# Kernel optimization log

Measured on AMD Instinct MI355X. Metric: run time of the kernel, lower is better.

The kernel has to match this reference:

```python
import jax, jax.numpy as jnp
import numpy as np

N, F, OUT = 8192, 256, 256


def setup_inputs() -> dict:
    key = jax.random.key(0)
    ks = jax.random.split(key, 8)
    s = 1.0 / np.sqrt(F)
    return {
        "features": jax.random.normal(ks[0], (N, F), jnp.float32),
        "key_features": jax.random.normal(ks[1], (N, F), jnp.float32),
        "adj_matrix": jax.random.uniform(ks[2], (N, N), jnp.float32),
        "W_d": jax.random.normal(ks[3], (2 * F, F), jnp.float32) * (1.0 / np.sqrt(2 * F)),
        "b_d": jnp.zeros((F,), jnp.float32),
        "W_o": jax.random.normal(ks[4], (F, OUT), jnp.float32) * s,
        "b_o": jnp.zeros((OUT,), jnp.float32),
        "W_a": jax.random.normal(ks[5], (F, F), jnp.float32) * s,
        "b_a": jnp.zeros((F,), jnp.float32),
        "W_ao": jax.random.normal(ks[6], (F, OUT), jnp.float32) * s,
        "b_ao": jnp.zeros((OUT,), jnp.float32),
    }


def reference(features, key_features, adj_matrix, W_d, b_d, W_o, b_o, W_a, b_a, W_ao, b_ao):
    n = features.shape[0]
    # masked softmax over rows; self-loop (diagonal) masked out
    neg = jnp.asarray(-1e9, adj_matrix.dtype)
    logits = adj_matrix * 5.0 + jnp.eye(n, dtype=adj_matrix.dtype) * neg
    a = jax.nn.softmax(logits, axis=-1)  # [N, N]
    # sum_j a_ij * concat(x_i, x_j) == concat(x_i * rowsum_i, (A @ X)_i)
    rowsum = jnp.sum(a, axis=-1, keepdims=True)  # == 1, kept for faithfulness
    agg = a @ features  # [N, F]
    neigh = jnp.concatenate([features * rowsum, agg], axis=-1)  # [N, 2F]
    neigh_distill = neigh @ W_d + b_d
    feature_updated = jnp.tanh((features - neigh_distill) @ W_o + b_o)
    # aggregate branch (withAgg=True)
    key_agg = (a @ key_features) @ W_a + b_a
    feature_aggregate = jnp.tanh((key_features + key_agg) @ W_ao + b_ao)
    return (feature_updated, feature_aggregate)
```

## Files before the change

kernel.cpp:

```cpp
#include <hip/hip_runtime.h>
#include <stdint.h>
#include <math.h>


typedef __attribute__((ext_vector_type(4)))  short bf16x4_t;
typedef __attribute__((ext_vector_type(8)))  short bf16x8_t;
typedef __attribute__((ext_vector_type(4)))  float f32x4_t;
typedef __attribute__((ext_vector_type(16))) float f32x16_t;

#define MFMA32(A, B, C) __builtin_amdgcn_mfma_f32_32x32x16_bf16(A, B, C, 0, 0, 0)
#define MFMA16(A, B, C) __builtin_amdgcn_mfma_f32_16x16x32_bf16(A, B, C, 0, 0, 0)

__device__ __forceinline__ unsigned short f2bf(float x) {
    union { float f; unsigned u; } c; c.f = x;
    unsigned u = c.u;
    return (unsigned short)((u + 0x7fffu + ((u >> 16) & 1u)) >> 16);
}
__device__ __forceinline__ unsigned pack2bf(float a, float b) {
    return (unsigned)f2bf(a) | ((unsigned)f2bf(b) << 16);
}
__device__ __forceinline__ float bflo(unsigned u) {
    union { unsigned u; float f; } c; c.u = u << 16; return c.f;
}
__device__ __forceinline__ float bfhi(unsigned u) {
    union { unsigned u; float f; } c; c.u = u & 0xffff0000u; return c.f;
}

__global__ __launch_bounds__(256) void transpose_f32_bf16(
    const float* __restrict__ src, unsigned short* __restrict__ dst, int R, int C)
{
    __shared__ float tile[32][33];
    const int x  = threadIdx.x & 31;
    const int y4 = (threadIdx.x >> 5) * 4;
    const int r0 = blockIdx.x * 32;
    const int c0 = blockIdx.y * 32;
#pragma unroll
    for (int i = 0; i < 4; ++i)
        tile[y4 + i][x] = src[(size_t)(r0 + y4 + i) * C + c0 + x];
    __syncthreads();
#pragma unroll
    for (int i = 0; i < 4; ++i)
        dst[(size_t)(c0 + y4 + i) * R + r0 + x] = f2bf(tile[x][y4 + i]);
}

__global__ __launch_bounds__(256) void pack_half(
    const float* __restrict__ src, unsigned* __restrict__ dst)
{
    const int idx = blockIdx.x * 256 + threadIdx.x;
    const int row = idx >> 7, cp = idx & 127;
    float2 v = *(const float2*)(src + (size_t)row * 256 + cp * 2);
    dst[(size_t)row * 256 + cp] = pack2bf(v.x, v.y);
}

__global__ __launch_bounds__(256) void compose1(
    const float* __restrict__ W_d, const float* __restrict__ W_o,
    unsigned short* __restrict__ W1t)
{
    __shared__ float wrow[256];
    const int k = blockIdx.x, t = threadIdx.x;
    wrow[t] = W_d[(size_t)k * 256 + t];
    __syncthreads();
    float acc = 0.f;
#pragma unroll 8
    for (int m = 0; m < 256; ++m) acc = fmaf(wrow[m], W_o[(size_t)m * 256 + t], acc);
    const float v = (k < 256 ? W_o[(size_t)k * 256 + t] : 0.f) - acc;
    W1t[(size_t)t * 512 + k] = f2bf(v);
}

__global__ __launch_bounds__(256) void compose2(
    const float* __restrict__ W_a, const float* __restrict__ W_ao,
    unsigned short* __restrict__ W2t)
{
    __shared__ float wrow[256];
    const int k = blockIdx.x, t = threadIdx.x;
    float v;
    if (k < 256) {
        v = W_ao[(size_t)k * 256 + t];
    } else {
        wrow[t] = W_a[(size_t)(k - 256) * 256 + t];
        __syncthreads();
        float acc = 0.f;
#pragma unroll 8
        for (int m = 0; m < 256; ++m) acc = fmaf(wrow[m], W_ao[(size_t)m * 256 + t], acc);
        v = acc;
    }
    W2t[(size_t)t * 512 + k] = f2bf(v);
}

__global__ __launch_bounds__(256) void biasC(
    const float* __restrict__ b_d, const float* __restrict__ b_o,
    const float* __restrict__ b_a, const float* __restrict__ b_ao,
    const float* __restrict__ W_o, const float* __restrict__ W_ao,
    float* __restrict__ c1, float* __restrict__ c2)
{
    const int t = threadIdx.x;
    float a1 = 0.f, a2 = 0.f;
#pragma unroll 8
    for (int m = 0; m < 256; ++m) {
        a1 = fmaf(b_d[m], W_o [(size_t)m * 256 + t], a1);
        a2 = fmaf(b_a[m], W_ao[(size_t)m * 256 + t], a2);
    }
    c1[t] = b_o[t] - a1;
    c2[t] = b_ao[t] + a2;
}

#define ROWS 128
#define KSLICE 2048
#define NIT 64
#define NCH 16
#define ASTRIDE 36

__global__ __launch_bounds__(1024) void exp_gemm(
    const float* __restrict__ adj, const unsigned short* __restrict__ Xt,
    unsigned* __restrict__ UpartB, float* __restrict__ sSp)
{
    __shared__ unsigned short sA[2][4][ROWS * ASTRIDE];

    const int t = threadIdx.x;
    const int w = t >> 6, lane = t & 63, q = lane >> 5, l31 = lane & 31;
    const int rb = blockIdx.x >> 2, h = blockIdx.x & 3;
    const int row0 = rb * ROWS, kbase = h * KSLICE;

    const int srow = t >> 3, skoff = (t & 7) * 4;
    const int sgrow = row0 + srow;
    const float* adj_row = adj + (size_t)sgrow * 8192 + kbase + skoff;
    const int swoff = srow * ASTRIDE + skoff;

    const unsigned short* bptr = Xt + (size_t)(w * 32 + l31) * 8192 + kbase + q * 8;

    float rs = 0.f;
    f32x16_t acc[4];
#pragma unroll
    for (int mt = 0; mt < 4; ++mt)
#pragma unroll
        for (int e = 0; e < 16; ++e) acc[mt][e] = 0.f;

    bf16x8_t bq[4][2];
    float4 qaA[4], qaB[4];

    auto stageChunk = [&](int cidx, const float4 (&qa)[4], int buf) {
        unsigned short* sb = &sA[buf][0][0] + swoff;
#pragma unroll
        for (int ks = 0; ks < 4; ++ks) {
            const float4 v = qa[ks];
            float e0 = __expf(5.f * v.x);
            float e1 = __expf(5.f * v.y);
            float e2 = __expf(5.f * v.z);
            float e3 = __expf(5.f * v.w);
            const int gk = kbase + (cidx * 4 + ks) * 32 + skoff;
            if (gk + 0 == sgrow) e0 = 0.f;
            if (gk + 1 == sgrow) e1 = 0.f;
            if (gk + 2 == sgrow) e2 = 0.f;
            if (gk + 3 == sgrow) e3 = 0.f;
            rs += (e0 + e1) + (e2 + e3);
            uint2 p; p.x = pack2bf(e0, e1); p.y = pack2bf(e2, e3);
            *(uint2*)(sb + ks * (ROWS * ASTRIDE)) = p;
        }
    };

    auto phase = [&](int c, float4 (&qaPre)[4], const float4 (&qaStg)[4], int buf) {
        if (c + 2 < NCH) {
#pragma unroll
            for (int ks = 0; ks < 4; ++ks)
                qaPre[ks] = *(const float4*)(adj_row + (size_t)((c + 2) * 4 + ks) * 32);
        }
        if (c + 1 < NCH) stageChunk(c + 1, qaStg, buf ^ 1);
#pragma unroll
        for (int u = 0; u < 4; ++u) {
            const int j = c * 4 + u;
            int jn = j + 2; if (jn >= NIT) jn = 0;
            bq[(u + 2) & 3][0] = *(const bf16x8_t*)(bptr + (size_t)jn * 32);
            bq[(u + 2) & 3][1] = *(const bf16x8_t*)(bptr + (size_t)jn * 32 + 16);
            const unsigned short* sa = &sA[buf][u][0] + l31 * ASTRIDE + q * 8;
#pragma unroll
            for (int s = 0; s < 2; ++s)
#pragma unroll
                for (int mt = 0; mt < 4; ++mt) {
                    const unsigned short* p = sa + mt * (32 * ASTRIDE) + s * 16;
                    bf16x4_t lo = *(const bf16x4_t*)p;
                    bf16x4_t hi = *(const bf16x4_t*)(p + 4);
                    bf16x8_t a = __builtin_shufflevector(lo, hi, 0, 1, 2, 3, 4, 5, 6, 7);
                    acc[mt] = MFMA32(a, bq[u][s], acc[mt]);
                }
        }
        asm volatile("s_waitcnt lgkmcnt(0)\n\ts_barrier" ::: "memory");
    };

#pragma unroll
    for (int ks = 0; ks < 4; ++ks)
        qaA[ks] = *(const float4*)(adj_row + (size_t)ks * 32);
#pragma unroll
    for (int ks = 0; ks < 4; ++ks)
        qaB[ks] = *(const float4*)(adj_row + (size_t)(4 + ks) * 32);
    stageChunk(0, qaA, 0);
    bq[0][0] = *(const bf16x8_t*)(bptr + 0);
    bq[0][1] = *(const bf16x8_t*)(bptr + 16);
    bq[1][0] = *(const bf16x8_t*)(bptr + 32);
    bq[1][1] = *(const bf16x8_t*)(bptr + 48);
    asm volatile("s_waitcnt lgkmcnt(0)\n\ts_barrier" ::: "memory");

    for (int c0 = 0; c0 < NCH; c0 += 2) {
        phase(c0,     qaA, qaB, 0);
        phase(c0 + 1, qaB, qaA, 1);
    }

    rs += __shfl_xor(rs, 1);
    rs += __shfl_xor(rs, 2);
    rs += __shfl_xor(rs, 4);
    if ((t & 7) == 0) sSp[h * 8192 + sgrow] = rs;

    unsigned* up = UpartB + (((size_t)h * 64 + rb) * 16 + w) * 2048 + lane;
#pragma unroll
    for (int mt = 0; mt < 4; ++mt)
#pragma unroll
        for (int ip = 0; ip < 8; ++ip)
            up[(size_t)(mt * 8 + ip) * 64] = pack2bf(acc[mt][2 * ip], acc[mt][2 * ip + 1]);
}

__global__ __launch_bounds__(256) void finalize_agg(
    const unsigned* __restrict__ UpartB, const float* __restrict__ sSp,
    unsigned* __restrict__ XcatN, unsigned* __restrict__ Kcat)
{
    __shared__ float sT[128][65];
    __shared__ float sInv[128];

    const int t = threadIdx.x;
    const int rb = blockIdx.x >> 3, wp = blockIdx.x & 7;
    const int row0 = rb * 128;

    if (t < 128) {
        const int r = row0 + t;
        sInv[t] = 1.f / (sSp[r] + sSp[8192 + r] + sSp[16384 + r] + sSp[24576 + r]);
    }

    const int i = t >> 3;
    const int l0 = (t & 7) * 8;
    const int mt = i >> 3, ip = i & 7;
    const int qq = l0 >> 5;
    const int rlo = mt * 32 + 2 * (ip & 1) + 8 * (ip >> 1) + 4 * qq;
    const int cbase = l0 & 31;

#pragma unroll
    for (int wi = 0; wi < 2; ++wi) {
        const int wv = wp * 2 + wi;
        float lo[8], hi[8];
#pragma unroll
        for (int j = 0; j < 8; ++j) { lo[j] = 0.f; hi[j] = 0.f; }
#pragma unroll
        for (int h = 0; h < 4; ++h) {
            const unsigned* src = UpartB + (((size_t)h * 64 + rb) * 16 + wv) * 2048
                                  + (size_t)i * 64 + l0;
            const uint4 v0 = *(const uint4*)(src);
            const uint4 v1 = *(const uint4*)(src + 4);
            const unsigned vv[8] = { v0.x, v0.y, v0.z, v0.w, v1.x, v1.y, v1.z, v1.w };
#pragma unroll
            for (int j = 0; j < 8; ++j) { lo[j] += bflo(vv[j]); hi[j] += bfhi(vv[j]); }
        }
#pragma unroll
        for (int j = 0; j < 8; ++j) {
            sT[rlo][wi * 32 + cbase + j]     = lo[j];
            sT[rlo + 1][wi * 32 + cbase + j] = hi[j];
        }
    }
    __syncthreads();

    const int row = t >> 1, cg = (t & 1) * 32;
    const float inv = sInv[row];
    unsigned outv[16];
#pragma unroll
    for (int j = 0; j < 16; ++j)
        outv[j] = pack2bf(sT[row][cg + 2 * j] * inv, sT[row][cg + 2 * j + 1] * inv);
    unsigned* dst = (wp < 4 ? XcatN : Kcat)
                    + (size_t)(row0 + row) * 256 + 128 + (wp & 3) * 32 + (cg >> 1);
#pragma unroll
    for (int j = 0; j < 4; ++j)
        *(uint4*)(dst + 4 * j) = *(const uint4*)(outv + 4 * j);
}

__global__ __launch_bounds__(256) void gemm_out(
    const unsigned short* __restrict__ Aa, const unsigned short* __restrict__ Wta,
    const float* __restrict__ ca,
    const unsigned short* __restrict__ Ab, const unsigned short* __restrict__ Wtb,
    const float* __restrict__ cb,
    float* __restrict__ outa, float* __restrict__ outb)
{
    __shared__ unsigned short sAm[16 * ASTRIDE];
    __shared__ unsigned short sB[256 * ASTRIDE];
    __shared__ float sBias[256];

    const int bid = blockIdx.x;
    const int prob = bid >> 9, tile = bid & 511;
    const unsigned short* A  = prob ? Ab  : Aa;
    const unsigned short* Wt = prob ? Wtb : Wta;
    const float* cvec        = prob ? cb  : ca;
    float* out               = prob ? outb : outa;

    const int t = threadIdx.x, w = t >> 6, lane = t & 63;
    const int m_lo = lane & 15, quad = lane >> 4;
    const int row0 = tile * 16;
    sBias[t] = cvec[t];

    f32x4_t acc[4];
#pragma unroll
    for (int b = 0; b < 4; ++b)
#pragma unroll
        for (int e = 0; e < 4; ++e) acc[b][e] = 0.f;

    for (int ks = 0; ks < 16; ++ks) {
        const int k0 = ks * 32;
        __syncthreads();
        if (t < 64) {
            bf16x8_t v = *(const bf16x8_t*)(A + (size_t)(row0 + (t >> 2)) * 512 + k0 + (t & 3) * 8);
            unsigned short* d = &sAm[(t >> 2) * ASTRIDE + (t & 3) * 8];
            *(bf16x4_t*)d       = __builtin_shufflevector(v, v, 0, 1, 2, 3);
            *(bf16x4_t*)(d + 4) = __builtin_shufflevector(v, v, 4, 5, 6, 7);
        }
        {
            const unsigned short* src = Wt + (size_t)t * 512 + k0;
            unsigned short* d = &sB[t * ASTRIDE];
#pragma unroll
            for (int j = 0; j < 4; ++j) {
                bf16x8_t v = *(const bf16x8_t*)(src + j * 8);
                *(bf16x4_t*)(d + j * 8)     = __builtin_shufflevector(v, v, 0, 1, 2, 3);
                *(bf16x4_t*)(d + j * 8 + 4) = __builtin_shufflevector(v, v, 4, 5, 6, 7);
            }
        }
        __syncthreads();
        bf16x8_t a0;
        {
            const unsigned short* p = &sAm[m_lo * ASTRIDE + quad * 8];
            bf16x4_t lo = *(const bf16x4_t*)p, hi = *(const bf16x4_t*)(p + 4);
            a0 = __builtin_shufflevector(lo, hi, 0, 1, 2, 3, 4, 5, 6, 7);
        }
#pragma unroll
        for (int nt = 0; nt < 4; ++nt) {
            const unsigned short* p = &sB[(w * 64 + nt * 16 + m_lo) * ASTRIDE + quad * 8];
            bf16x4_t lo = *(const bf16x4_t*)p, hi = *(const bf16x4_t*)(p + 4);
            bf16x8_t b = __builtin_shufflevector(lo, hi, 0, 1, 2, 3, 4, 5, 6, 7);
            acc[nt] = MFMA16(a0, b, acc[nt]);
        }
    }

#pragma unroll
    for (int nt = 0; nt < 4; ++nt) {
        const int col = w * 64 + nt * 16 + m_lo;
#pragma unroll
        for (int r = 0; r < 4; ++r) {
            const int row = row0 + quad * 4 + r;
            out[(size_t)row * 256 + col] = tanhf(acc[nt][r] + sBias[col]);
        }
    }
}

extern "C" void kernel_launch(void* const* d_in, const int* in_sizes, int n_in,
                              void* d_out, int out_size, void* d_ws, size_t ws_size,
                              hipStream_t stream) {
    const float* features = (const float*)d_in[0];
    const float* key      = (const float*)d_in[1];
    const float* adj      = (const float*)d_in[2];
    const float* W_d  = (const float*)d_in[3];
    const float* b_d  = (const float*)d_in[4];
    const float* W_o  = (const float*)d_in[5];
    const float* b_o  = (const float*)d_in[6];
    const float* W_a  = (const float*)d_in[7];
    const float* b_a  = (const float*)d_in[8];
    const float* W_ao = (const float*)d_in[9];
    const float* b_ao = (const float*)d_in[10];

    float* out1 = (float*)d_out;
    float* out2 = out1 + (size_t)8192 * 256;

    char* ws = (char*)d_ws;
    unsigned short* XcatN = (unsigned short*)(ws);
    unsigned short* Kcat  = (unsigned short*)(ws +  8388608);
    unsigned short* Xt    = (unsigned short*)(ws + 16777216);
    unsigned*       UpartB= (unsigned*)      (ws + 25165824);
    float*          sSp   = (float*)         (ws + 58720256);
    unsigned short* W1t   = (unsigned short*)(ws + 58851328);
    unsigned short* W2t   = (unsigned short*)(ws + 59113472);
    float*          c1    = (float*)         (ws + 59375616);
    float*          c2    = (float*)         (ws + 59376640);

    dim3 blk(256);
    transpose_f32_bf16<<<dim3(256, 8), blk, 0, stream>>>(features, Xt, 8192, 256);
    transpose_f32_bf16<<<dim3(256, 8), blk, 0, stream>>>(key, Xt + (size_t)256 * 8192, 8192, 256);
    pack_half<<<4096, blk, 0, stream>>>(features, (unsigned*)XcatN);
    pack_half<<<4096, blk, 0, stream>>>(key, (unsigned*)Kcat);
    compose1<<<512, blk, 0, stream>>>(W_d, W_o, W1t);
    compose2<<<512, blk, 0, stream>>>(W_a, W_ao, W2t);
    biasC<<<1, blk, 0, stream>>>(b_d, b_o, b_a, b_ao, W_o, W_ao, c1, c2);

    exp_gemm<<<256, dim3(1024), 0, stream>>>(adj, Xt, UpartB, sSp);
    finalize_agg<<<512, blk, 0, stream>>>(UpartB, sSp,
                                          (unsigned*)XcatN, (unsigned*)Kcat);

    gemm_out<<<1024, blk, 0, stream>>>(XcatN, W1t, c1, Kcat, W2t, c2, out1, out2);
}
```

Baseline: 596.9 us.

## Pre-swizzle X into MFMA fragment blobs and retile exp_gemm to 64-row blocks

The transpose kernel now writes X/key into a blob layout matching MFMA B-fragment order, so exp_gemm's B loads become contiguous 16-byte per-lane reads. exp_gemm drops to 64 rows per block with 512 threads and 2x2 32x32 tiles per wave, giving twice as many blocks and higher occupancy via launch bounds, plus s_setprio around the MFMA groups. finalize_agg and gemm_out are resized to match, and gemm_out now computes 32 rows per block to reuse the B tile. This trades reuse of staged adj tiles per block for more parallelism and cheaper B fetches.

```diff
diff --git a/kernel.cpp b/kernel.cpp
--- a/kernel.cpp
+++ b/kernel.cpp
@@ -26,21 +26,25 @@
     union { unsigned u; float f; } c; c.u = u & 0xffff0000u; return c.f;
 }
 
-__global__ __launch_bounds__(256) void transpose_f32_bf16(
-    const float* __restrict__ src, unsigned short* __restrict__ dst, int R, int C)
+__global__ __launch_bounds__(256) void transpose_blob(
+    const float* __restrict__ src, unsigned short* __restrict__ Xtb, int c32base)
 {
     __shared__ float tile[32][33];
-    const int x  = threadIdx.x & 31;
-    const int y4 = (threadIdx.x >> 5) * 4;
-    const int r0 = blockIdx.x * 32;
-    const int c0 = blockIdx.y * 32;
+    const int t = threadIdx.x;
+    const int x = t & 31, y4 = (t >> 5) * 4;
+    const int r0 = blockIdx.x * 32, c0 = blockIdx.y * 32;
 #pragma unroll
     for (int i = 0; i < 4; ++i)
-        tile[y4 + i][x] = src[(size_t)(r0 + y4 + i) * C + c0 + x];
+        tile[y4 + i][x] = src[(size_t)(r0 + y4 + i) * 256 + c0 + x];
     __syncthreads();
-#pragma unroll
-    for (int i = 0; i < 4; ++i)
-        dst[(size_t)(c0 + y4 + i) * R + r0 + x] = f2bf(tile[x][y4 + i]);
+    const int s = t >> 7, lane = (t >> 1) & 63, e0 = (t & 1) * 4;
+    const int kl = s * 16 + (lane >> 5) * 8 + e0;
+    const int cl = lane & 31;
+    unsigned short* blob = Xtb + ((size_t)blockIdx.x * 16 + (c0 >> 5) + c32base) * 1024;
+    uint2 v;
+    v.x = pack2bf(tile[kl][cl],     tile[kl + 1][cl]);
+    v.y = pack2bf(tile[kl + 2][cl], tile[kl + 3][cl]);
+    *(uint2*)(blob + t * 4) = v;
 }
 
 __global__ __launch_bounds__(256) void pack_half(
@@ -104,14 +108,14 @@
     c2[t] = b_ao[t] + a2;
 }
 
-#define ROWS 128
+#define ROWS 64
 #define KSLICE 2048
 #define NIT 64
 #define NCH 16
 #define ASTRIDE 36
 
-__global__ __launch_bounds__(1024) void exp_gemm(
-    const float* __restrict__ adj, const unsigned short* __restrict__ Xt,
+__global__ __launch_bounds__(512, 4) void exp_gemm(
+    const float* __restrict__ adj, const unsigned short* __restrict__ Xtb,
     unsigned* __restrict__ UpartB, float* __restrict__ sSp)
 {
     __shared__ unsigned short sA[2][4][ROWS * ASTRIDE];
@@ -119,23 +123,26 @@
     const int t = threadIdx.x;
     const int w = t >> 6, lane = t & 63, q = lane >> 5, l31 = lane & 31;
     const int rb = blockIdx.x >> 2, h = blockIdx.x & 3;
-    const int row0 = rb * ROWS, kbase = h * KSLICE;
+    const int row0 = rb * ROWS;
+    const int kbase = h * KSLICE, jbase = h * (KSLICE / 32);
 
     const int srow = t >> 3, skoff = (t & 7) * 4;
     const int sgrow = row0 + srow;
     const float* adj_row = adj + (size_t)sgrow * 8192 + kbase + skoff;
     const int swoff = srow * ASTRIDE + skoff;
 
-    const unsigned short* bptr = Xt + (size_t)(w * 32 + l31) * 8192 + kbase + q * 8;
+    const unsigned short* wb = Xtb + (size_t)(2 * w) * 1024 + lane * 8;
 
     float rs = 0.f;
-    f32x16_t acc[4];
-#pragma unroll
-    for (int mt = 0; mt < 4; ++mt)
-#pragma unroll
-        for (int e = 0; e < 16; ++e) acc[mt][e] = 0.f;
-
-    bf16x8_t bq[4][2];
+    f32x16_t acc[2][2];
+#pragma unroll
+    for (int mt = 0; mt < 2; ++mt)
+#pragma unroll
+        for (int ct = 0; ct < 2; ++ct)
+#pragma unroll
+            for (int e = 0; e < 16; ++e) acc[mt][ct][e] = 0.f;
+
+    bf16x8_t bq[2][2][4];
     float4 qaA[4], qaB[4];
 
     auto stageChunk = [&](int cidx, const float4 (&qa)[4], int buf) {
@@ -169,19 +176,30 @@
         for (int u = 0; u < 4; ++u) {
             const int j = c * 4 + u;
             int jn = j + 2; if (jn >= NIT) jn = 0;
-            bq[(u + 2) & 3][0] = *(const bf16x8_t*)(bptr + (size_t)jn * 32);
-            bq[(u + 2) & 3][1] = *(const bf16x8_t*)(bptr + (size_t)jn * 32 + 16);
+            const unsigned short* bb = wb + (size_t)(jbase + jn) * 16384;
+#pragma unroll
+            for (int k4 = 0; k4 < 4; ++k4)
+                bq[((u >> 1) ^ 1) & 1][u & 1][k4] = *(const bf16x8_t*)(bb + k4 * 512);
             const unsigned short* sa = &sA[buf][u][0] + l31 * ASTRIDE + q * 8;
-#pragma unroll
-            for (int s = 0; s < 2; ++s)
-#pragma unroll
-                for (int mt = 0; mt < 4; ++mt) {
+            bf16x8_t af[2][2];
+#pragma unroll
+            for (int mt = 0; mt < 2; ++mt)
+#pragma unroll
+                for (int s = 0; s < 2; ++s) {
                     const unsigned short* p = sa + mt * (32 * ASTRIDE) + s * 16;
                     bf16x4_t lo = *(const bf16x4_t*)p;
                     bf16x4_t hi = *(const bf16x4_t*)(p + 4);
-                    bf16x8_t a = __builtin_shufflevector(lo, hi, 0, 1, 2, 3, 4, 5, 6, 7);
-                    acc[mt] = MFMA32(a, bq[u][s], acc[mt]);
+                    af[mt][s] = __builtin_shufflevector(lo, hi, 0, 1, 2, 3, 4, 5, 6, 7);
                 }
+            __builtin_amdgcn_s_setprio(1);
+#pragma unroll
+            for (int s = 0; s < 2; ++s)
+#pragma unroll
+                for (int mt = 0; mt < 2; ++mt)
+#pragma unroll
+                    for (int ct = 0; ct < 2; ++ct)
+                        acc[mt][ct] = MFMA32(af[mt][s], bq[(u >> 1) & 1][u & 1][ct * 2 + s], acc[mt][ct]);
+            __builtin_amdgcn_s_setprio(0);
         }
         asm volatile("s_waitcnt lgkmcnt(0)\n\ts_barrier" ::: "memory");
     };
@@ -193,10 +211,15 @@
     for (int ks = 0; ks < 4; ++ks)
         qaB[ks] = *(const float4*)(adj_row + (size_t)(4 + ks) * 32);
     stageChunk(0, qaA, 0);
-    bq[0][0] = *(const bf16x8_t*)(bptr + 0);
-    bq[0][1] = *(const bf16x8_t*)(bptr + 16);
-    bq[1][0] = *(const bf16x8_t*)(bptr + 32);
-    bq[1][1] = *(const bf16x8_t*)(bptr + 48);
+    {
+        const unsigned short* b0 = wb + (size_t)(jbase + 0) * 16384;
+        const unsigned short* b1 = wb + (size_t)(jbase + 1) * 16384;
+#pragma unroll
+        for (int k4 = 0; k4 < 4; ++k4) {
+            bq[0][0][k4] = *(const bf16x8_t*)(b0 + k4 * 512);
+            bq[0][1][k4] = *(const bf16x8_t*)(b1 + k4 * 512);
+        }
+    }
     asm volatile("s_waitcnt lgkmcnt(0)\n\ts_barrier" ::: "memory");
 
     for (int c0 = 0; c0 < NCH; c0 += 2) {
@@ -209,72 +232,70 @@
     rs += __shfl_xor(rs, 4);
     if ((t & 7) == 0) sSp[h * 8192 + sgrow] = rs;
 
-    unsigned* up = UpartB + (((size_t)h * 64 + rb) * 16 + w) * 2048 + lane;
-#pragma unroll
-    for (int mt = 0; mt < 4; ++mt)
-#pragma unroll
-        for (int ip = 0; ip < 8; ++ip)
-            up[(size_t)(mt * 8 + ip) * 64] = pack2bf(acc[mt][2 * ip], acc[mt][2 * ip + 1]);
+    unsigned* up = UpartB + (((size_t)h * 128 + rb) * 8 + w) * 2048 + lane;
+#pragma unroll
+    for (int mt = 0; mt < 2; ++mt)
+#pragma unroll
+        for (int ct = 0; ct < 2; ++ct)
+#pragma unroll
+            for (int ip = 0; ip < 8; ++ip)
+                up[(size_t)(((mt * 2 + ct) * 8) + ip) * 64] =
+                    pack2bf(acc[mt][ct][2 * ip], acc[mt][ct][2 * ip + 1]);
 }
 
 __global__ __launch_bounds__(256) void finalize_agg(
     const unsigned* __restrict__ UpartB, const float* __restrict__ sSp,
     unsigned* __restrict__ XcatN, unsigned* __restrict__ Kcat)
 {
-    __shared__ float sT[128][65];
-    __shared__ float sInv[128];
+    __shared__ float sT[64][65];
+    __shared__ float sInv[64];
 
     const int t = threadIdx.x;
     const int rb = blockIdx.x >> 3, wp = blockIdx.x & 7;
-    const int row0 = rb * 128;
-
-    if (t < 128) {
+    const int row0 = rb * 64;
+
+    if (t < 64) {
         const int r = row0 + t;
         sInv[t] = 1.f / (sSp[r] + sSp[8192 + r] + sSp[16384 + r] + sSp[24576 + r]);
     }
 
     const int i = t >> 3;
     const int l0 = (t & 7) * 8;
-    const int mt = i >> 3, ip = i & 7;
+    const int mt = i >> 4, ct = (i >> 3) & 1, ip = i & 7;
     const int qq = l0 >> 5;
     const int rlo = mt * 32 + 2 * (ip & 1) + 8 * (ip >> 1) + 4 * qq;
-    const int cbase = l0 & 31;
-
-#pragma unroll
-    for (int wi = 0; wi < 2; ++wi) {
-        const int wv = wp * 2 + wi;
-        float lo[8], hi[8];
-#pragma unroll
-        for (int j = 0; j < 8; ++j) { lo[j] = 0.f; hi[j] = 0.f; }
-#pragma unroll
-        for (int h = 0; h < 4; ++h) {
-            const unsigned* src = UpartB + (((size_t)h * 64 + rb) * 16 + wv) * 2048
-                                  + (size_t)i * 64 + l0;
-            const uint4 v0 = *(const uint4*)(src);
-            const uint4 v1 = *(const uint4*)(src + 4);
-            const unsigned vv[8] = { v0.x, v0.y, v0.z, v0.w, v1.x, v1.y, v1.z, v1.w };
-#pragma unroll
-            for (int j = 0; j < 8; ++j) { lo[j] += bflo(vv[j]); hi[j] += bfhi(vv[j]); }
-        }
-#pragma unroll
-        for (int j = 0; j < 8; ++j) {
-            sT[rlo][wi * 32 + cbase + j]     = lo[j];
-            sT[rlo + 1][wi * 32 + cbase + j] = hi[j];
-        }
+    const int cbase = ct * 32 + (l0 & 31);
+
+    float lo[8], hi[8];
+#pragma unroll
+    for (int j = 0; j < 8; ++j) { lo[j] = 0.f; hi[j] = 0.f; }
+#pragma unroll
+    for (int h = 0; h < 4; ++h) {
+        const unsigned* src = UpartB + (((size_t)h * 128 + rb) * 8 + wp) * 2048
+                              + (size_t)i * 64 + l0;
+        const uint4 v0 = *(const uint4*)(src);
+        const uint4 v1 = *(const uint4*)(src + 4);
+        const unsigned vv[8] = { v0.x, v0.y, v0.z, v0.w, v1.x, v1.y, v1.z, v1.w };
+#pragma unroll
+        for (int j = 0; j < 8; ++j) { lo[j] += bflo(vv[j]); hi[j] += bfhi(vv[j]); }
+    }
+#pragma unroll
+    for (int j = 0; j < 8; ++j) {
+        sT[rlo][cbase + j]     = lo[j];
+        sT[rlo + 1][cbase + j] = hi[j];
     }
     __syncthreads();
 
-    const int row = t >> 1, cg = (t & 1) * 32;
+    const int row = t >> 2, cg = (t & 3) * 16;
     const float inv = sInv[row];
-    unsigned outv[16];
-#pragma unroll
-    for (int j = 0; j < 16; ++j)
+    unsigned outv[8];
+#pragma unroll
+    for (int j = 0; j < 8; ++j)
         outv[j] = pack2bf(sT[row][cg + 2 * j] * inv, sT[row][cg + 2 * j + 1] * inv);
     unsigned* dst = (wp < 4 ? XcatN : Kcat)
                     + (size_t)(row0 + row) * 256 + 128 + (wp & 3) * 32 + (cg >> 1);
-#pragma unroll
-    for (int j = 0; j < 4; ++j)
-        *(uint4*)(dst + 4 * j) = *(const uint4*)(outv + 4 * j);
+    *(uint4*)(dst)     = *(const uint4*)(outv);
+    *(uint4*)(dst + 4) = *(const uint4*)(outv + 4);
 }
 
 __global__ __launch_bounds__(256) void gemm_out(
@@ -284,12 +305,12 @@
     const float* __restrict__ cb,
     float* __restrict__ outa, float* __restrict__ outb)
 {
-    __shared__ unsigned short sAm[16 * ASTRIDE];
+    __shared__ unsigned short sAm[32 * ASTRIDE];
     __shared__ unsigned short sB[256 * ASTRIDE];
     __shared__ float sBias[256];
 
     const int bid = blockIdx.x;
-    const int prob = bid >> 9, tile = bid & 511;
+    const int prob = bid >> 8, tile = bid & 255;
     const unsigned short* A  = prob ? Ab  : Aa;
     const unsigned short* Wt = prob ? Wtb : Wta;
     const float* cvec        = prob ? cb  : ca;
@@ -297,19 +318,21 @@
 
     const int t = threadIdx.x, w = t >> 6, lane = t & 63;
     const int m_lo = lane & 15, quad = lane >> 4;
-    const int row0 = tile * 16;
+    const int row0 = tile * 32;
     sBias[t] = cvec[t];
 
-    f32x4_t acc[4];
-#pragma unroll
-    for (int b = 0; b < 4; ++b)
-#pragma unroll
-        for (int e = 0; e < 4; ++e) acc[b][e] = 0.f;
+    f32x4_t acc[2][4];
+#pragma unroll
+    for (int a = 0; a < 2; ++a)
+#pragma unroll
+        for (int b = 0; b < 4; ++b)
+#pragma unroll
+            for (int e = 0; e < 4; ++e) acc[a][b][e] = 0.f;
 
     for (int ks = 0; ks < 16; ++ks) {
         const int k0 = ks * 32;
         __syncthreads();
-        if (t < 64) {
+        if (t < 128) {
             bf16x8_t v = *(const bf16x8_t*)(A + (size_t)(row0 + (t >> 2)) * 512 + k0 + (t & 3) * 8);
             unsigned short* d = &sAm[(t >> 2) * ASTRIDE + (t & 3) * 8];
             *(bf16x4_t*)d       = __builtin_shufflevector(v, v, 0, 1, 2, 3);
@@ -326,30 +349,36 @@
             }
         }
         __syncthreads();
-        bf16x8_t a0;
+        bf16x8_t a0, a1;
         {
             const unsigned short* p = &sAm[m_lo * ASTRIDE + quad * 8];
             bf16x4_t lo = *(const bf16x4_t*)p, hi = *(const bf16x4_t*)(p + 4);
             a0 = __builtin_shufflevector(lo, hi, 0, 1, 2, 3, 4, 5, 6, 7);
+            p += 16 * ASTRIDE;
+            lo = *(const bf16x4_t*)p; hi = *(const bf16x4_t*)(p + 4);
+            a1 = __builtin_shufflevector(lo, hi, 0, 1, 2, 3, 4, 5, 6, 7);
         }
 #pragma unroll
         for (int nt = 0; nt < 4; ++nt) {
             const unsigned short* p = &sB[(w * 64 + nt * 16 + m_lo) * ASTRIDE + quad * 8];
             bf16x4_t lo = *(const bf16x4_t*)p, hi = *(const bf16x4_t*)(p + 4);
             bf16x8_t b = __builtin_shufflevector(lo, hi, 0, 1, 2, 3, 4, 5, 6, 7);
-            acc[nt] = MFMA16(a0, b, acc[nt]);
-        }
-    }
-
-#pragma unroll
-    for (int nt = 0; nt < 4; ++nt) {
-        const int col = w * 64 + nt * 16 + m_lo;
-#pragma unroll
-        for (int r = 0; r < 4; ++r) {
-            const int row = row0 + quad * 4 + r;
-            out[(size_t)row * 256 + col] = tanhf(acc[nt][r] + sBias[col]);
-        }
-    }
+            acc[0][nt] = MFMA16(a0, b, acc[0][nt]);
+            acc[1][nt] = MFMA16(a1, b, acc[1][nt]);
+        }
+    }
+
+#pragma unroll
+    for (int mt = 0; mt < 2; ++mt)
+#pragma unroll
+        for (int nt = 0; nt < 4; ++nt) {
+            const int col = w * 64 + nt * 16 + m_lo;
+#pragma unroll
+            for (int r = 0; r < 4; ++r) {
+                const int row = row0 + mt * 16 + quad * 4 + r;
+                out[(size_t)row * 256 + col] = tanhf(acc[mt][nt][r] + sBias[col]);
+            }
+        }
 }
 
 extern "C" void kernel_launch(void* const* d_in, const int* in_sizes, int n_in,
@@ -373,7 +402,7 @@
     char* ws = (char*)d_ws;
     unsigned short* XcatN = (unsigned short*)(ws);
     unsigned short* Kcat  = (unsigned short*)(ws +  8388608);
-    unsigned short* Xt    = (unsigned short*)(ws + 16777216);
+    unsigned short* Xtb   = (unsigned short*)(ws + 16777216);
     unsigned*       UpartB= (unsigned*)      (ws + 25165824);
     float*          sSp   = (float*)         (ws + 58720256);
     unsigned short* W1t   = (unsigned short*)(ws + 58851328);
@@ -382,17 +411,17 @@
     float*          c2    = (float*)         (ws + 59376640);
 
     dim3 blk(256);
-    transpose_f32_bf16<<<dim3(256, 8), blk, 0, stream>>>(features, Xt, 8192, 256);
-    transpose_f32_bf16<<<dim3(256, 8), blk, 0, stream>>>(key, Xt + (size_t)256 * 8192, 8192, 256);
+    transpose_blob<<<dim3(256, 8), blk, 0, stream>>>(features, Xtb, 0);
+    transpose_blob<<<dim3(256, 8), blk, 0, stream>>>(key, Xtb, 8);
     pack_half<<<4096, blk, 0, stream>>>(features, (unsigned*)XcatN);
     pack_half<<<4096, blk, 0, stream>>>(key, (unsigned*)Kcat);
     compose1<<<512, blk, 0, stream>>>(W_d, W_o, W1t);
     compose2<<<512, blk, 0, stream>>>(W_a, W_ao, W2t);
     biasC<<<1, blk, 0, stream>>>(b_d, b_o, b_a, b_ao, W_o, W_ao, c1, c2);
 
-    exp_gemm<<<256, dim3(1024), 0, stream>>>(adj, Xt, UpartB, sSp);
-    finalize_agg<<<512, blk, 0, stream>>>(UpartB, sSp,
-                                          (unsigned*)XcatN, (unsigned*)Kcat);
-
-    gemm_out<<<1024, blk, 0, stream>>>(XcatN, W1t, c1, Kcat, W2t, c2, out1, out2);
-}
+    exp_gemm<<<512, dim3(512), 0, stream>>>(adj, Xtb, UpartB, sSp);
+    finalize_agg<<<1024, blk, 0, stream>>>(UpartB, sSp,
+                                           (unsigned*)XcatN, (unsigned*)Kcat);
+
+    gemm_out<<<512, blk, 0, stream>>>(XcatN, W1t, c1, Kcat, W2t, c2, out1, out2);
+}
```

Measured after the change: 835.0 us. +39.9%, slower.
